# Optimization experiments

Measured on AMD Instinct MI355X. Metric: run time of the kernel, lower is better.

Reference implementation:

```python
import jax, jax.numpy as jnp
import numpy as np

ALPHA = 0.2  # LeakyReLU negative slope

def setup_inputs() -> dict:
    key = jax.random.key(0)
    k1, k2, k3 = jax.random.split(key, 3)
    N, S, D = 8192, 64, 128  # groups, neighbors per group, feature dim
    center_feature = jax.random.normal(k1, (N, S, D), dtype=jnp.float32)
    nbr_feature = jax.random.normal(k2, (N, S, D), dtype=jnp.float32)
    # xavier_uniform_ on (2D, 1) with gain=1.414: bound = gain*sqrt(6/(2D+1))
    bound = 1.414 * np.sqrt(6.0 / (2 * D + 1))
    a = jax.random.uniform(k3, (2 * D, 1), dtype=jnp.float32, minval=-bound, maxval=bound)
    return {"center_feature": center_feature, "nbr_feature": nbr_feature, "a": a}

def reference(center_feature, nbr_feature, a):
    D = center_feature.shape[-1]
    # cat([c, n]) @ a == c @ a[:D] + n @ a[D:]  (avoid materializing the concat)
    e = center_feature @ a[:D] + nbr_feature @ a[D:]      # [N, S, 1]
    e = jax.nn.leaky_relu(e, negative_slope=ALPHA)
    attention = jax.nn.softmax(e, axis=1)                  # softmax over neighbors
    # dropout is identity in eval mode (training=False)
    graph_pooling = jnp.sum(attention * nbr_feature, axis=1)  # [N, D]
    return graph_pooling
```

## Files before the change

kernel.cpp:

```cpp
#include <hip/hip_runtime.h>
#include <math.h>

#define ALPHA 0.2f
#define S_DIM 64
#define D_DIM 128
#define TILE_F4 2048

__global__ __launch_bounds__(256) void gat_fused_kernel(
    const float* __restrict__ center,
    const float* __restrict__ nbr,
    const float* __restrict__ a,
    float* __restrict__ out)
{
    const int n = blockIdx.x;
    const int t = threadIdx.x;
    const int c = t & 31;
    const int g = t >> 5;
    const int d0 = c * 4;

    __shared__ float e_lds[S_DIM];
    __shared__ float att_lds[S_DIM];
    __shared__ float out_lds[8 * D_DIM];

    const float4* c4p = (const float4*)(center + (size_t)n * (S_DIM * D_DIM));
    const float4* n4p = (const float4*)(nbr    + (size_t)n * (S_DIM * D_DIM));

    const float4 a0 = *(const float4*)(a + d0);
    const float4 a1 = *(const float4*)(a + D_DIM + d0);

    float4 nv[8];
    float partial[8];
#pragma unroll
    for (int k = 0; k < 8; ++k) {
        const int f = t + 256 * k;
        const float4 cv = c4p[f];
        const float4 nk = n4p[f];
        nv[k] = nk;
        partial[k] = cv.x * a0.x + cv.y * a0.y + cv.z * a0.z + cv.w * a0.w
                   + nk.x * a1.x + nk.y * a1.y + nk.z * a1.z + nk.w * a1.w;
    }

#pragma unroll
    for (int k = 0; k < 8; ++k) {
        float v = partial[k];
        v += __shfl_xor(v, 16);
        v += __shfl_xor(v, 8);
        v += __shfl_xor(v, 4);
        v += __shfl_xor(v, 2);
        v += __shfl_xor(v, 1);
        if (c == 0) e_lds[g + 8 * k] = v;
    }
    __syncthreads();

    if (t < 64) {
        float v = e_lds[t];
        v = (v > 0.0f) ? v : ALPHA * v;
        float m = v;
        m = fmaxf(m, __shfl_xor(m, 32));
        m = fmaxf(m, __shfl_xor(m, 16));
        m = fmaxf(m, __shfl_xor(m, 8));
        m = fmaxf(m, __shfl_xor(m, 4));
        m = fmaxf(m, __shfl_xor(m, 2));
        m = fmaxf(m, __shfl_xor(m, 1));
        const float ex = expf(v - m);
        float sum = ex;
        sum += __shfl_xor(sum, 32);
        sum += __shfl_xor(sum, 16);
        sum += __shfl_xor(sum, 8);
        sum += __shfl_xor(sum, 4);
        sum += __shfl_xor(sum, 2);
        sum += __shfl_xor(sum, 1);
        att_lds[t] = ex / sum;
    }
    __syncthreads();

    float4 o = make_float4(0.f, 0.f, 0.f, 0.f);
#pragma unroll
    for (int k = 0; k < 8; ++k) {
        const float w = att_lds[g + 8 * k];
        o.x += w * nv[k].x;
        o.y += w * nv[k].y;
        o.z += w * nv[k].z;
        o.w += w * nv[k].w;
    }
    *(float4*)(out_lds + g * D_DIM + d0) = o;
    __syncthreads();

    if (t < 32) {
        float4 s = make_float4(0.f, 0.f, 0.f, 0.f);
#pragma unroll
        for (int gg = 0; gg < 8; ++gg) {
            const float4 v = *(const float4*)(out_lds + gg * D_DIM + t * 4);
            s.x += v.x; s.y += v.y; s.z += v.z; s.w += v.w;
        }
        *(float4*)(out + (size_t)n * D_DIM + t * 4) = s;
    }
}

extern "C" void kernel_launch(void* const* d_in, const int* in_sizes, int n_in,
                              void* d_out, int out_size, void* d_ws, size_t ws_size,
                              hipStream_t stream) {
    const float* center = (const float*)d_in[0];
    const float* nbr    = (const float*)d_in[1];
    const float* a      = (const float*)d_in[2];
    float* out = (float*)d_out;

    int N;
    if (n_in >= 3 && in_sizes[2] > 0) {
        N = (in_sizes[0] / in_sizes[2]) / 32;
    } else {
        N = in_sizes[0] / (S_DIM * D_DIM);
    }
    if (N < 1) N = 1;

    gat_fused_kernel<<<N, 256, 0, stream>>>(center, nbr, a, out);
}
```

Baseline: 501.8 us.

## Process four groups per block with register prefetch of the next group

Each block now handles four consecutive groups and issues the global loads for the next group into registers before running the current group's reduction, softmax and pooling. This is meant to hide memory latency behind the syncthreads-heavy compute phase and to reduce block launch overhead. It raises register pressure from the extra prefetch buffers, which may lower occupancy, and cuts the grid to a quarter of its former size.

After: 509.2 us. About the same (+1.5%).

```diff
diff --git a/kernel.cpp b/kernel.cpp
--- a/kernel.cpp
+++ b/kernel.cpp
@@ -4,96 +4,125 @@
 #define ALPHA 0.2f
 #define S_DIM 64
 #define D_DIM 128
-#define TILE_F4 2048
+#define GPB 4
 
 __global__ __launch_bounds__(256) void gat_fused_kernel(
     const float* __restrict__ center,
     const float* __restrict__ nbr,
     const float* __restrict__ a,
-    float* __restrict__ out)
+    float* __restrict__ out,
+    int n_total)
 {
-    const int n = blockIdx.x;
     const int t = threadIdx.x;
     const int c = t & 31;
     const int g = t >> 5;
     const int d0 = c * 4;
+    const int n0 = blockIdx.x * GPB;
 
     __shared__ float e_lds[S_DIM];
     __shared__ float att_lds[S_DIM];
     __shared__ float out_lds[8 * D_DIM];
 
-    const float4* c4p = (const float4*)(center + (size_t)n * (S_DIM * D_DIM));
-    const float4* n4p = (const float4*)(nbr    + (size_t)n * (S_DIM * D_DIM));
-
     const float4 a0 = *(const float4*)(a + d0);
     const float4 a1 = *(const float4*)(a + D_DIM + d0);
 
-    float4 nv[8];
-    float partial[8];
+    float4 cv[8];
+    float4 nv[8], nv2[8];
+
+    {
+        const float4* c4p = (const float4*)(center + (size_t)n0 * (S_DIM * D_DIM));
+        const float4* n4p = (const float4*)(nbr    + (size_t)n0 * (S_DIM * D_DIM));
 #pragma unroll
-    for (int k = 0; k < 8; ++k) {
-        const int f = t + 256 * k;
-        const float4 cv = c4p[f];
-        const float4 nk = n4p[f];
-        nv[k] = nk;
-        partial[k] = cv.x * a0.x + cv.y * a0.y + cv.z * a0.z + cv.w * a0.w
-                   + nk.x * a1.x + nk.y * a1.y + nk.z * a1.z + nk.w * a1.w;
+        for (int k = 0; k < 8; ++k) {
+            const int f = t + 256 * k;
+            cv[k] = c4p[f];
+            nv[k] = n4p[f];
+        }
     }
 
+#pragma unroll 1
+    for (int i = 0; i < GPB; ++i) {
+        const int n = n0 + i;
+        if (n >= n_total) break;
+
+        float partial[8];
 #pragma unroll
-    for (int k = 0; k < 8; ++k) {
-        float v = partial[k];
-        v += __shfl_xor(v, 16);
-        v += __shfl_xor(v, 8);
-        v += __shfl_xor(v, 4);
-        v += __shfl_xor(v, 2);
-        v += __shfl_xor(v, 1);
-        if (c == 0) e_lds[g + 8 * k] = v;
-    }
-    __syncthreads();
+        for (int k = 0; k < 8; ++k) {
+            partial[k] = cv[k].x * a0.x + cv[k].y * a0.y + cv[k].z * a0.z + cv[k].w * a0.w
+                       + nv[k].x * a1.x + nv[k].y * a1.y + nv[k].z * a1.z + nv[k].w * a1.w;
+        }
 
-    if (t < 64) {
-        float v = e_lds[t];
-        v = (v > 0.0f) ? v : ALPHA * v;
-        float m = v;
-        m = fmaxf(m, __shfl_xor(m, 32));
-        m = fmaxf(m, __shfl_xor(m, 16));
-        m = fmaxf(m, __shfl_xor(m, 8));
-        m = fmaxf(m, __shfl_xor(m, 4));
-        m = fmaxf(m, __shfl_xor(m, 2));
-        m = fmaxf(m, __shfl_xor(m, 1));
-        const float ex = expf(v - m);
-        float sum = ex;
-        sum += __shfl_xor(sum, 32);
-        sum += __shfl_xor(sum, 16);
-        sum += __shfl_xor(sum, 8);
-        sum += __shfl_xor(sum, 4);
-        sum += __shfl_xor(sum, 2);
-        sum += __shfl_xor(sum, 1);
-        att_lds[t] = ex / sum;
-    }
-    __syncthreads();
+        if (i + 1 < GPB && n + 1 < n_total) {
+            const float4* c4p = (const float4*)(center + (size_t)(n + 1) * (S_DIM * D_DIM));
+            const float4* n4p = (const float4*)(nbr    + (size_t)(n + 1) * (S_DIM * D_DIM));
+#pragma unroll
+            for (int k = 0; k < 8; ++k) {
+                const int f = t + 256 * k;
+                cv[k]  = c4p[f];
+                nv2[k] = n4p[f];
+            }
+        }
 
-    float4 o = make_float4(0.f, 0.f, 0.f, 0.f);
 #pragma unroll
-    for (int k = 0; k < 8; ++k) {
-        const float w = att_lds[g + 8 * k];
-        o.x += w * nv[k].x;
-        o.y += w * nv[k].y;
-        o.z += w * nv[k].z;
-        o.w += w * nv[k].w;
-    }
-    *(float4*)(out_lds + g * D_DIM + d0) = o;
-    __syncthreads();
+        for (int k = 0; k < 8; ++k) {
+            float v = partial[k];
+            v += __shfl_xor(v, 16);
+            v += __shfl_xor(v, 8);
+            v += __shfl_xor(v, 4);
+            v += __shfl_xor(v, 2);
+            v += __shfl_xor(v, 1);
+            if (c == 0) e_lds[g + 8 * k] = v;
+        }
+        __syncthreads();
 
-    if (t < 32) {
-        float4 s = make_float4(0.f, 0.f, 0.f, 0.f);
+        if (t < 64) {
+            float v = e_lds[t];
+            v = (v > 0.0f) ? v : ALPHA * v;
+            float m = v;
+            m = fmaxf(m, __shfl_xor(m, 32));
+            m = fmaxf(m, __shfl_xor(m, 16));
+            m = fmaxf(m, __shfl_xor(m, 8));
+            m = fmaxf(m, __shfl_xor(m, 4));
+            m = fmaxf(m, __shfl_xor(m, 2));
+            m = fmaxf(m, __shfl_xor(m, 1));
+            const float ex = expf(v - m);
+            float sum = ex;
+            sum += __shfl_xor(sum, 32);
+            sum += __shfl_xor(sum, 16);
+            sum += __shfl_xor(sum, 8);
+            sum += __shfl_xor(sum, 4);
+            sum += __shfl_xor(sum, 2);
+            sum += __shfl_xor(sum, 1);
+            att_lds[t] = ex / sum;
+        }
+        __syncthreads();
+
+        float4 o = make_float4(0.f, 0.f, 0.f, 0.f);
 #pragma unroll
-        for (int gg = 0; gg < 8; ++gg) {
-            const float4 v = *(const float4*)(out_lds + gg * D_DIM + t * 4);
-            s.x += v.x; s.y += v.y; s.z += v.z; s.w += v.w;
+        for (int k = 0; k < 8; ++k) {
+            const float w = att_lds[g + 8 * k];
+            o.x += w * nv[k].x;
+            o.y += w * nv[k].y;
+            o.z += w * nv[k].z;
+            o.w += w * nv[k].w;
         }
-        *(float4*)(out + (size_t)n * D_DIM + t * 4) = s;
+        *(float4*)(out_lds + g * D_DIM + d0) = o;
+        __syncthreads();
+
+        if (t < 32) {
+            float4 s = make_float4(0.f, 0.f, 0.f, 0.f);
+#pragma unroll
+            for (int gg = 0; gg < 8; ++gg) {
+                const float4 v = *(const float4*)(out_lds + gg * D_DIM + t * 4);
+                s.x += v.x; s.y += v.y; s.z += v.z; s.w += v.w;
+            }
+            *(float4*)(out + (size_t)n * D_DIM + t * 4) = s;
+        }
+
+        if (i + 1 < GPB) {
+#pragma unroll
+            for (int k = 0; k < 8; ++k) nv[k] = nv2[k];
+        }
     }
 }
 
@@ -113,5 +142,6 @@
     }
     if (N < 1) N = 1;
 
-    gat_fused_kernel<<<N, 256, 0, stream>>>(center, nbr, a, out);
+    const int grid = (N + GPB - 1) / GPB;
+    gat_fused_kernel<<<grid, 256, 0, stream>>>(center, nbr, a, out, N);
 }
```
